# Performance work log

Hardware: AMD Instinct MI355X
Metric: run time of the kernel (lower is better)

Reference implementation:

```python
import jax, jax.numpy as jnp
import numpy as np

KERNEL_BANDWIDTH = 0.3
STEP_SIZE = 0.5
NB_ITERATIONS = 4


def setup_inputs() -> dict:
    key = jax.random.key(0)
    # B x D x H x W pixel embeddings
    x_in = jax.random.normal(key, (2, 64, 96, 96), dtype=jnp.float32)
    return {"x_in": x_in}


def reference(x_in):
    B, D, H, W = x_in.shape
    N = H * W
    x0 = x_in.reshape(B, D, N)

    def body(x, _):
        # Gaussian-like kernel K[i,j] = exp(bw * <x_i, x_j>), symmetric NxN per batch
        K = jnp.exp(KERNEL_BANDWIDTH * jnp.einsum('bdn,bdm->bnm', x, x))  # (B,N,N)
        # torch: diag(K^T @ 1) then inverse of that diagonal == 1/column-sums
        colsum = jnp.sum(K, axis=1)  # (B,N)
        # x @ (K diag(1/colsum)): column-normalized weighted mean of embeddings
        xk = jnp.einsum('bdn,bnm->bdm', x, K) / colsum[:, None, :]
        x_new = STEP_SIZE * xk + (1.0 - STEP_SIZE) * x
        return x_new, x_new

    _, ys = jax.lax.scan(body, x0, None, length=NB_ITERATIONS)  # (I,B,D,N)
    allx = jnp.concatenate([x0[None], ys], axis=0)  # (I+1,B,D,N)
    # B x (I+1) x D x H x W
    return jnp.transpose(allx, (1, 0, 2, 3)).reshape(B, NB_ITERATIONS + 1, D, H, W)
```

## Files before the change

### kernel.cpp

```cpp
#include <hip/hip_runtime.h>
#include <hip/hip_bf16.h>

constexpr int B_    = 2;
constexpr int D_    = 64;
constexpr int N_    = 9216;
constexpr int ITERS = 4;

constexpr int MTQ     = 128;
constexpr int MBF     = N_ / MTQ;
constexpr int KS      = 4;
constexpr int KEYS_WG = N_ / KS;
constexpr int KTILES  = KEYS_WG / 128;
constexpr int NWG     = B_ * MBF * KS;
constexpr int PB      = 144;

constexpr float KBW  = 0.3f;
constexpr float STEP = 0.5f;
constexpr float C2   = 0.43280851226668905f;

using short8   = __attribute__((ext_vector_type(8))) short;
using float16v = __attribute__((ext_vector_type(16))) float;
typedef __attribute__((ext_vector_type(2))) __bf16 bf16x2;

__device__ __forceinline__ unsigned short f2bf(float f) {
  union { float f; unsigned u; } v; v.f = f;
  unsigned u = v.u;
  unsigned r = (u + 0x7fffu + ((u >> 16) & 1u)) >> 16;
  return (unsigned short)r;
}

#if __has_builtin(__builtin_amdgcn_cvt_pk_bf16_f32)
__device__ __forceinline__ unsigned pk2bf(float a, float b) {
  bf16x2 r = __builtin_amdgcn_cvt_pk_bf16_f32(a, b);
  union { bf16x2 h; unsigned u; } v; v.h = r; return v.u;
}
#else
__device__ __forceinline__ unsigned pk2bf(float a, float b) {
  return (unsigned)f2bf(a) | ((unsigned)f2bf(b) << 16);
}
#endif

__device__ __forceinline__ float csum2(unsigned u, float cs) {
#if __has_builtin(__builtin_amdgcn_fdot2_f32_bf16)
  union { unsigned x; bf16x2 h; } a, o;
  a.x = u; o.x = 0x3f803f80u;
  return __builtin_amdgcn_fdot2_f32_bf16(a.h, o.h, cs, false);
#else
  union { unsigned u; float f; } lo, hi;
  lo.u = u << 16; hi.u = u & 0xffff0000u;
  return cs + lo.f + hi.f;
#endif
}

__device__ __forceinline__ void dma16(const unsigned short* g,
                                      unsigned short* lds_base, int lane) {
#if __has_builtin(__builtin_amdgcn_global_load_lds)
  __builtin_amdgcn_global_load_lds(
      (const __attribute__((address_space(1))) unsigned int*)g,
      (__attribute__((address_space(3))) unsigned int*)lds_base, 16, 0, 0);
#else
  *(int4*)((char*)lds_base + lane * 16) = *(const int4*)g;
#endif
}

__global__ void prep_kernel(const float* __restrict__ xin, float* __restrict__ out,
                            unsigned short* __restrict__ XT,
                            unsigned short* __restrict__ Xbf)
{
  const int bx = blockIdx.x;
  const int nb = bx % PB, b = bx / PB;
  const int n0 = nb * 64;
  const int tid = threadIdx.x;
  __shared__ float tile[64 * 65];

  #pragma unroll
  for (int r = 0; r < 16; ++r) {
    int idx = r * 256 + tid;
    int d = idx >> 6, j = idx & 63;
    float v = xin[((size_t)b * 64 + d) * N_ + n0 + j];
    out[(((size_t)b * 5 + 0) * 64 + d) * N_ + n0 + j] = v;
    Xbf[((size_t)b * 64 + d) * N_ + n0 + j] = f2bf(v);
    tile[d * 65 + j] = v;
  }
  __syncthreads();
  #pragma unroll
  for (int r = 0; r < 16; ++r) {
    int idx = r * 256 + tid;
    int nl = idx >> 6, d = idx & 63;
    XT[((size_t)b * N_ + n0 + nl) * 64 + d] = f2bf(tile[d * 65 + nl]);
  }
}

__global__ void __launch_bounds__(256, 3) flash_kernel(
    const unsigned short* __restrict__ XT,
    const unsigned short* __restrict__ Xbf,
    float* __restrict__ pacc, float* __restrict__ pcs)
{
  const int bx   = blockIdx.x;
  const int ks   = bx & 3;
  const int mb   = (bx >> 2) % MBF;
  const int b    = bx / (MBF * KS);
  const int tid  = threadIdx.x;
  const int wave = tid >> 6, lane = tid & 63;
  const int c = lane & 31, h = lane >> 5;
  const int cp = (c & 0x13) | ((c & 4) << 1) | ((c & 8) >> 1);
  const int m0 = mb * MTQ;
  const int bpaddr = (lane ^ 32) << 2;

  const unsigned short* XTb = XT  + (size_t)b * N_ * 64;
  const unsigned short* Xb  = Xbf + (size_t)b * 64 * N_;

  __shared__ unsigned short sXT[128 * 64];
  __shared__ unsigned short sXB[64 * 128];

  short8 qf[4];
  #pragma unroll
  for (int k = 0; k < 4; ++k) {
    short8 raw = *(const short8*)(XTb +
        (size_t)(m0 + wave * 32 + c) * 64 + k * 16 + h * 8);
    unsigned o[4];
    const unsigned* rw = (const unsigned*)&raw;
    #pragma unroll
    for (int p4 = 0; p4 < 4; ++p4) {
      union { unsigned u; float f; } lo, hi;
      lo.u = rw[p4] << 16; hi.u = rw[p4] & 0xffff0000u;
      o[p4] = pk2bf(lo.f * C2, hi.f * C2);
    }
    qf[k] = *(const short8*)o;
  }

  float16v zv;
  #pragma unroll
  for (int p = 0; p < 16; ++p) zv[p] = 0.f;
  float16v acc[2];
  acc[0] = zv; acc[1] = zv;
  float cs = 0.f;

  const int xt_rr = lane >> 3, xt_sc = lane & 7;
  const int xb_rr = lane >> 4, xb_sc = lane & 15;

  int n0g = ks * KEYS_WG;
  for (int t = 0; t < KTILES; ++t, n0g += 128) {
    __syncthreads();
    #pragma unroll
    for (int ii = 0; ii < 4; ++ii) {
      int row = wave * 32 + ii * 8 + xt_rr;
      int gc  = xt_sc ^ (row & 7);
      dma16(XTb + (size_t)(n0g + row) * 64 + gc * 8,
            sXT + (wave * 32 + ii * 8) * 64, lane);
    }
    #pragma unroll
    for (int ii = 0; ii < 4; ++ii) {
      int row = wave * 16 + ii * 4 + xb_rr;
      int gc  = xb_sc ^ (row & 7);
      dma16(Xb + (size_t)row * N_ + n0g + gc * 8,
            sXB + (wave * 16 + ii * 4) * 128, lane);
    }
    __syncthreads();

    #pragma unroll
    for (int s = 0; s < 4; ++s) {
      short8 af[4];
      #pragma unroll
      for (int k = 0; k < 4; ++k)
        af[k] = *(const short8*)(sXT + (s * 32 + cp) * 64 +
                                 ((k * 2 + h) ^ (cp & 7)) * 8);

      float16v S = zv;
      #pragma unroll
      for (int k = 0; k < 4; ++k)
        S = __builtin_amdgcn_mfma_f32_32x32x16_bf16(af[k], qf[k], S, 0, 0, 0);

      unsigned q[8];
      #pragma unroll
      for (int g = 0; g < 8; ++g) {
        float w0 = __builtin_amdgcn_exp2f(S[2 * g]);
        float w1 = __builtin_amdgcn_exp2f(S[2 * g + 1]);
        unsigned u = pk2bf(w0, w1);
        q[g] = u;
        cs = csum2(u, cs);
      }

      union { unsigned d[4]; short8 s; } a20, a21;
      a20.d[0] = q[0]; a20.d[1] = q[1]; a20.d[2] = q[2]; a20.d[3] = q[3];
      a21.d[0] = q[4]; a21.d[1] = q[5]; a21.d[2] = q[6]; a21.d[3] = q[7];

      short8 b20[2], b21[2];
      #pragma unroll
      for (int dt = 0; dt < 2; ++dt) {
        b20[dt] = *(const short8*)(sXB + (dt * 32 + c) * 128 + ((4 * s + h)     ^ (c & 7)) * 8);
        b21[dt] = *(const short8*)(sXB + (dt * 32 + c) * 128 + ((4 * s + 2 + h) ^ (c & 7)) * 8);
      }
      #pragma unroll
      for (int dt = 0; dt < 2; ++dt)
        acc[dt] = __builtin_amdgcn_mfma_f32_32x32x16_bf16(a20.s, b20[dt], acc[dt], 0, 0, 0);
      #pragma unroll
      for (int dt = 0; dt < 2; ++dt)
        acc[dt] = __builtin_amdgcn_mfma_f32_32x32x16_bf16(a21.s, b21[dt], acc[dt], 0, 0, 0);
    }
  }

  union { float f; int i; } cu; cu.f = cs;
  cu.i = __builtin_amdgcn_ds_bpermute(bpaddr, cu.i);
  float cst = cs + cu.f;
  if (h == 0) pcs[(size_t)bx * 128 + wave * 32 + c] = cst;

  float* pw = pacc + (size_t)bx * (MTQ * 64);
  #pragma unroll
  for (int dt = 0; dt < 2; ++dt)
    #pragma unroll
    for (int p = 0; p < 16; ++p) {
      int m = wave * 32 + (p & 3) + 8 * (p >> 2) + 4 * h;
      pw[m * 64 + dt * 32 + c] = acc[dt][p];
    }
}

__global__ void combine_kernel(const float* __restrict__ pacc,
                               const float* __restrict__ pcs,
                               float* __restrict__ out,
                               unsigned short* __restrict__ XT,
                               unsigned short* __restrict__ Xbf, int t)
{
  const int bx = blockIdx.x;
  const int mb = bx % MBF, b = bx / MBF;
  const int m0 = mb * MTQ;
  const int tid = threadIdx.x;
  __shared__ float accs[128 * 65];
  __shared__ float cst[128];
  const int base = (b * MBF + mb) * KS;

  #pragma unroll
  for (int r = 0; r < 32; ++r) {
    int idx = r * 256 + tid;
    float s = 0.f;
    #pragma unroll
    for (int k = 0; k < KS; ++k) s += pacc[(size_t)(base + k) * 8192 + idx];
    accs[(idx >> 6) * 65 + (idx & 63)] = s;
  }
  if (tid < 128) {
    float cv = 0.f;
    #pragma unroll
    for (int k = 0; k < KS; ++k) cv += pcs[(size_t)(base + k) * 128 + tid];
    cst[tid] = cv;
  }
  __syncthreads();

  #pragma unroll
  for (int r = 0; r < 32; ++r) {
    int idx = r * 256 + tid;
    int m = idx & 127, d = idx >> 7;
    float a = accs[m * 65 + d];
    size_t obase = (((size_t)b * 5 + t) * 64 + d) * N_ + m0 + m;
    float xc = out[obase];
    float v = STEP * (a / cst[m]) + (1.f - STEP) * xc;
    out[obase + (size_t)64 * N_] = v;
    Xbf[((size_t)b * 64 + d) * N_ + m0 + m] = f2bf(v);
    accs[m * 65 + d] = v;
  }
  __syncthreads();

  #pragma unroll
  for (int r = 0; r < 32; ++r) {
    int idx = r * 256 + tid;
    int m = idx >> 6, d = idx & 63;
    XT[((size_t)b * N_ + m0 + m) * 64 + d] = f2bf(accs[m * 65 + d]);
  }
}

extern "C" void kernel_launch(void* const* d_in, const int* in_sizes, int n_in,
                              void* d_out, int out_size, void* d_ws, size_t ws_size,
                              hipStream_t stream)
{
  (void)in_sizes; (void)n_in; (void)out_size; (void)ws_size;
  const float* xin = (const float*)d_in[0];
  float* out = (float*)d_out;
  char* ws = (char*)d_ws;

  unsigned short* XT  = (unsigned short*)(ws);
  unsigned short* Xbf = (unsigned short*)(ws +  2359296);
  float*          pacc = (float*)(ws +  4718592);
  float*          pcs  = (float*)(ws + 23592960);

  prep_kernel<<<B_ * PB, 256, 0, stream>>>(xin, out, XT, Xbf);
  for (int t = 0; t < ITERS; ++t) {
    flash_kernel<<<NWG, 256, 0, stream>>>(XT, Xbf, pacc, pcs);
    combine_kernel<<<B_ * MBF, 256, 0, stream>>>(pacc, pcs, out, XT, Xbf, t);
  }
}
```

Measured before the change: 418.4 us.

## Double query tile per workgroup and reduce key-split partials with float atomics

Each flash workgroup now handles 256 queries, two 32-row tiles per wave, so every loaded key tile in shared memory feeds twice as many MFMAs. The key dimension is split 9 ways instead of 4. Partial sums and column sums are accumulated into a single zeroed global buffer with atomicAdd instead of per-split partial buffers, so combine just reads one result. This costs a memset per iteration, heavy float atomic traffic, more registers (occupancy hint lowered to 2), and nondeterministic summation order.

```diff
diff --git a/kernel.cpp b/kernel.cpp
--- a/kernel.cpp
+++ b/kernel.cpp
@@ -6,13 +6,15 @@
 constexpr int N_    = 9216;
 constexpr int ITERS = 4;
 
-constexpr int MTQ     = 128;
+constexpr int MTQ     = 256;
 constexpr int MBF     = N_ / MTQ;
-constexpr int KS      = 4;
+constexpr int KS      = 9;
 constexpr int KEYS_WG = N_ / KS;
 constexpr int KTILES  = KEYS_WG / 128;
 constexpr int NWG     = B_ * MBF * KS;
 constexpr int PB      = 144;
+constexpr int CBM     = 128;
+constexpr int CB      = N_ / CBM;
 
 constexpr float KBW  = 0.3f;
 constexpr float STEP = 0.5f;
@@ -91,15 +93,16 @@
   }
 }
 
-__global__ void __launch_bounds__(256, 3) flash_kernel(
+__global__ void __launch_bounds__(256, 2) flash_kernel(
     const unsigned short* __restrict__ XT,
     const unsigned short* __restrict__ Xbf,
-    float* __restrict__ pacc, float* __restrict__ pcs)
+    float* __restrict__ accG, float* __restrict__ csG)
 {
   const int bx   = blockIdx.x;
-  const int ks   = bx & 3;
-  const int mb   = (bx >> 2) % MBF;
-  const int b    = bx / (MBF * KS);
+  const int ks   = bx % KS;
+  const int rest = bx / KS;
+  const int mb   = rest % MBF;
+  const int b    = rest / MBF;
   const int tid  = threadIdx.x;
   const int wave = tid >> 6, lane = tid & 63;
   const int c = lane & 31, h = lane >> 5;
@@ -113,28 +116,30 @@
   __shared__ unsigned short sXT[128 * 64];
   __shared__ unsigned short sXB[64 * 128];
 
-  short8 qf[4];
-  #pragma unroll
-  for (int k = 0; k < 4; ++k) {
-    short8 raw = *(const short8*)(XTb +
-        (size_t)(m0 + wave * 32 + c) * 64 + k * 16 + h * 8);
-    unsigned o[4];
-    const unsigned* rw = (const unsigned*)&raw;
-    #pragma unroll
-    for (int p4 = 0; p4 < 4; ++p4) {
-      union { unsigned u; float f; } lo, hi;
-      lo.u = rw[p4] << 16; hi.u = rw[p4] & 0xffff0000u;
-      o[p4] = pk2bf(lo.f * C2, hi.f * C2);
-    }
-    qf[k] = *(const short8*)o;
-  }
+  short8 qf[2][4];
+  #pragma unroll
+  for (int mt = 0; mt < 2; ++mt)
+    #pragma unroll
+    for (int k = 0; k < 4; ++k) {
+      short8 raw = *(const short8*)(XTb +
+          (size_t)(m0 + wave * 64 + mt * 32 + c) * 64 + k * 16 + h * 8);
+      unsigned o[4];
+      const unsigned* rw = (const unsigned*)&raw;
+      #pragma unroll
+      for (int p4 = 0; p4 < 4; ++p4) {
+        union { unsigned u; float f; } lo, hi;
+        lo.u = rw[p4] << 16; hi.u = rw[p4] & 0xffff0000u;
+        o[p4] = pk2bf(lo.f * C2, hi.f * C2);
+      }
+      qf[mt][k] = *(const short8*)o;
+    }
 
   float16v zv;
   #pragma unroll
   for (int p = 0; p < 16; ++p) zv[p] = 0.f;
-  float16v acc[2];
-  acc[0] = zv; acc[1] = zv;
-  float cs = 0.f;
+  float16v acc[2][2];
+  acc[0][0] = zv; acc[0][1] = zv; acc[1][0] = zv; acc[1][1] = zv;
+  float cs[2] = {0.f, 0.f};
 
   const int xt_rr = lane >> 3, xt_sc = lane & 7;
   const int xb_rr = lane >> 4, xb_sc = lane & 15;
@@ -165,84 +170,83 @@
       for (int k = 0; k < 4; ++k)
         af[k] = *(const short8*)(sXT + (s * 32 + cp) * 64 +
                                  ((k * 2 + h) ^ (cp & 7)) * 8);
-
-      float16v S = zv;
-      #pragma unroll
-      for (int k = 0; k < 4; ++k)
-        S = __builtin_amdgcn_mfma_f32_32x32x16_bf16(af[k], qf[k], S, 0, 0, 0);
-
-      unsigned q[8];
-      #pragma unroll
-      for (int g = 0; g < 8; ++g) {
-        float w0 = __builtin_amdgcn_exp2f(S[2 * g]);
-        float w1 = __builtin_amdgcn_exp2f(S[2 * g + 1]);
-        unsigned u = pk2bf(w0, w1);
-        q[g] = u;
-        cs = csum2(u, cs);
-      }
-
-      union { unsigned d[4]; short8 s; } a20, a21;
-      a20.d[0] = q[0]; a20.d[1] = q[1]; a20.d[2] = q[2]; a20.d[3] = q[3];
-      a21.d[0] = q[4]; a21.d[1] = q[5]; a21.d[2] = q[6]; a21.d[3] = q[7];
-
       short8 b20[2], b21[2];
       #pragma unroll
       for (int dt = 0; dt < 2; ++dt) {
         b20[dt] = *(const short8*)(sXB + (dt * 32 + c) * 128 + ((4 * s + h)     ^ (c & 7)) * 8);
         b21[dt] = *(const short8*)(sXB + (dt * 32 + c) * 128 + ((4 * s + 2 + h) ^ (c & 7)) * 8);
       }
-      #pragma unroll
-      for (int dt = 0; dt < 2; ++dt)
-        acc[dt] = __builtin_amdgcn_mfma_f32_32x32x16_bf16(a20.s, b20[dt], acc[dt], 0, 0, 0);
-      #pragma unroll
-      for (int dt = 0; dt < 2; ++dt)
-        acc[dt] = __builtin_amdgcn_mfma_f32_32x32x16_bf16(a21.s, b21[dt], acc[dt], 0, 0, 0);
-    }
-  }
-
-  union { float f; int i; } cu; cu.f = cs;
-  cu.i = __builtin_amdgcn_ds_bpermute(bpaddr, cu.i);
-  float cst = cs + cu.f;
-  if (h == 0) pcs[(size_t)bx * 128 + wave * 32 + c] = cst;
-
-  float* pw = pacc + (size_t)bx * (MTQ * 64);
-  #pragma unroll
-  for (int dt = 0; dt < 2; ++dt)
-    #pragma unroll
-    for (int p = 0; p < 16; ++p) {
-      int m = wave * 32 + (p & 3) + 8 * (p >> 2) + 4 * h;
-      pw[m * 64 + dt * 32 + c] = acc[dt][p];
-    }
-}
-
-__global__ void combine_kernel(const float* __restrict__ pacc,
-                               const float* __restrict__ pcs,
+
+      #pragma unroll
+      for (int mt = 0; mt < 2; ++mt) {
+        float16v S = zv;
+        #pragma unroll
+        for (int k = 0; k < 4; ++k)
+          S = __builtin_amdgcn_mfma_f32_32x32x16_bf16(af[k], qf[mt][k], S, 0, 0, 0);
+
+        unsigned q[8];
+        #pragma unroll
+        for (int g = 0; g < 8; ++g) {
+          float w0 = __builtin_amdgcn_exp2f(S[2 * g]);
+          float w1 = __builtin_amdgcn_exp2f(S[2 * g + 1]);
+          unsigned u = pk2bf(w0, w1);
+          q[g] = u;
+          cs[mt] = csum2(u, cs[mt]);
+        }
+
+        union { unsigned d[4]; short8 s; } a20, a21;
+        a20.d[0] = q[0]; a20.d[1] = q[1]; a20.d[2] = q[2]; a20.d[3] = q[3];
+        a21.d[0] = q[4]; a21.d[1] = q[5]; a21.d[2] = q[6]; a21.d[3] = q[7];
+
+        #pragma unroll
+        for (int dt = 0; dt < 2; ++dt)
+          acc[mt][dt] = __builtin_amdgcn_mfma_f32_32x32x16_bf16(
+              a20.s, b20[dt], acc[mt][dt], 0, 0, 0);
+        #pragma unroll
+        for (int dt = 0; dt < 2; ++dt)
+          acc[mt][dt] = __builtin_amdgcn_mfma_f32_32x32x16_bf16(
+              a21.s, b21[dt], acc[mt][dt], 0, 0, 0);
+      }
+    }
+  }
+
+  #pragma unroll
+  for (int mt = 0; mt < 2; ++mt) {
+    union { float f; int i; } cu; cu.f = cs[mt];
+    cu.i = __builtin_amdgcn_ds_bpermute(bpaddr, cu.i);
+    float cst = cs[mt] + cu.f;
+    if (h == 0)
+      atomicAdd(&csG[(size_t)b * N_ + m0 + wave * 64 + mt * 32 + c], cst);
+    #pragma unroll
+    for (int dt = 0; dt < 2; ++dt)
+      #pragma unroll
+      for (int p = 0; p < 16; ++p) {
+        int m = m0 + wave * 64 + mt * 32 + (p & 3) + 8 * (p >> 2) + 4 * h;
+        atomicAdd(&accG[((size_t)b * N_ + m) * 64 + dt * 32 + c], acc[mt][dt][p]);
+      }
+  }
+}
+
+__global__ void combine_kernel(const float* __restrict__ accG,
+                               const float* __restrict__ csG,
                                float* __restrict__ out,
                                unsigned short* __restrict__ XT,
                                unsigned short* __restrict__ Xbf, int t)
 {
   const int bx = blockIdx.x;
-  const int mb = bx % MBF, b = bx / MBF;
-  const int m0 = mb * MTQ;
+  const int mb = bx % CB, b = bx / CB;
+  const int m0 = mb * CBM;
   const int tid = threadIdx.x;
   __shared__ float accs[128 * 65];
   __shared__ float cst[128];
-  const int base = (b * MBF + mb) * KS;
 
   #pragma unroll
   for (int r = 0; r < 32; ++r) {
     int idx = r * 256 + tid;
-    float s = 0.f;
-    #pragma unroll
-    for (int k = 0; k < KS; ++k) s += pacc[(size_t)(base + k) * 8192 + idx];
-    accs[(idx >> 6) * 65 + (idx & 63)] = s;
-  }
-  if (tid < 128) {
-    float cv = 0.f;
-    #pragma unroll
-    for (int k = 0; k < KS; ++k) cv += pcs[(size_t)(base + k) * 128 + tid];
-    cst[tid] = cv;
-  }
+    accs[(idx >> 6) * 65 + (idx & 63)] =
+        accG[((size_t)b * N_ + m0) * 64 + idx];
+  }
+  if (tid < 128) cst[tid] = csG[(size_t)b * N_ + m0 + tid];
   __syncthreads();
 
   #pragma unroll
@@ -276,14 +280,15 @@
   float* out = (float*)d_out;
   char* ws = (char*)d_ws;
 
-  unsigned short* XT  = (unsigned short*)(ws);
-  unsigned short* Xbf = (unsigned short*)(ws +  2359296);
-  float*          pacc = (float*)(ws +  4718592);
-  float*          pcs  = (float*)(ws + 23592960);
+  unsigned short* XT   = (unsigned short*)(ws);
+  unsigned short* Xbf  = (unsigned short*)(ws + 2359296);
+  float*          accG = (float*)(ws + 4718592);
+  float*          csG  = (float*)(ws + 9437184);
 
   prep_kernel<<<B_ * PB, 256, 0, stream>>>(xin, out, XT, Xbf);
   for (int t = 0; t < ITERS; ++t) {
-    flash_kernel<<<NWG, 256, 0, stream>>>(XT, Xbf, pacc, pcs);
-    combine_kernel<<<B_ * MBF, 256, 0, stream>>>(pacc, pcs, out, XT, Xbf, t);
-  }
-}
+    hipMemsetAsync(ws + 4718592, 0, 4718592 + 73728, stream);
+    flash_kernel<<<NWG, 256, 0, stream>>>(XT, Xbf, accG, csG);
+    combine_kernel<<<B_ * CB, 256, 0, stream>>>(accG, csG, out, XT, Xbf, t);
+  }
+}
```

Result: slower. 463.8 us (+10.8%).
